# Kernel tuning notes

Measured on AMD Instinct MI355X. Metric: run time of the kernel, lower is better.

## Reference

```python
import jax, jax.numpy as jnp
import numpy as np

N_NODES = 100000
N_EDGES = 1600000
IN_FEATS = 128
H_FEATS = 64
NUM_CLASSES = 40
NEG_SLOPE = 0.2  # DGL GATConv default


def gat_layer(x, src, dst, W, attn_l, attn_r, bias, n_nodes):
    # x: [N, din]; W: [din, dout]; attn_l/r, bias: [dout]
    feat = x @ W                                   # [N, dout]
    el = feat @ attn_l                             # [N]
    er = feat @ attn_r                             # [N]
    e = jax.nn.leaky_relu(el[src] + er[dst], NEG_SLOPE)  # [E]
    # segment softmax over destination nodes (numerically stable)
    m = jax.ops.segment_max(e, dst, num_segments=n_nodes)   # [N]
    ee = jnp.exp(e - m[dst])                                 # [E]
    s = jax.ops.segment_sum(ee, dst, num_segments=n_nodes)  # [N]
    alpha = ee / s[dst]                                      # [E]
    out = jax.ops.segment_sum(alpha[:, None] * feat[src], dst,
                              num_segments=n_nodes)          # [N, dout]
    return out + bias


def setup_inputs() -> dict:
    key = jax.random.key(0)
    ks = jax.random.split(key, 12)
    in_feat = jax.random.normal(ks[0], (N_NODES, IN_FEATS), dtype=jnp.float32)
    src = jax.random.randint(ks[1], (N_EDGES,), 0, N_NODES, dtype=jnp.int32)
    dst = jax.random.randint(ks[2], (N_EDGES,), 0, N_NODES, dtype=jnp.int32)
    def glorot(k, shape):
        fan = sum(shape)
        return jax.random.normal(k, shape, dtype=jnp.float32) * jnp.sqrt(2.0 / fan)
    W1 = glorot(ks[3], (IN_FEATS, H_FEATS))
    al1 = glorot(ks[4], (H_FEATS,)) 
    ar1 = glorot(ks[5], (H_FEATS,))
    b1 = jnp.zeros((H_FEATS,), jnp.float32)
    W2 = glorot(ks[6], (H_FEATS, NUM_CLASSES))
    al2 = glorot(ks[7], (NUM_CLASSES,))
    ar2 = glorot(ks[8], (NUM_CLASSES,))
    b2 = jnp.zeros((NUM_CLASSES,), jnp.float32)
    return {"in_feat": in_feat, "src": src, "dst": dst,
            "W1": W1, "al1": al1, "ar1": ar1, "b1": b1,
            "W2": W2, "al2": al2, "ar2": ar2, "b2": b2}


def reference(in_feat, src, dst, W1, al1, ar1, b1, W2, al2, ar2, b2):
    h = gat_layer(in_feat, src, dst, W1, al1, ar1, b1, N_NODES)  # gat1
    h = jax.nn.elu(h)                                            # F.elu
    h = gat_layer(h, src, dst, W2, al2, ar2, b2, N_NODES)        # gat2
    return h  # [N, num_classes]
```

## Files before the change

### kernel.cpp

```cpp
#include <hip/hip_runtime.h>

#define N_NODES 100000
#define N_EDGES 1600000
#define DB_SHIFT 9
#define DB_SIZE 512
#define NDB 196
#define DB_CAP 10240

constexpr float NEG_SLOPE = 0.2f;

__device__ __forceinline__ float leaky(float x) { return x > 0.f ? x : NEG_SLOPE * x; }

__device__ __forceinline__ float bflo(unsigned u) { return __uint_as_float(u << 16); }
__device__ __forceinline__ float bfhi(unsigned u) { return __uint_as_float(u & 0xffff0000u); }

__device__ __forceinline__ void bfsplit(float x, short& h, short& l) {
    unsigned u = __float_as_uint(x);
    h = (short)(u >> 16);
    float res = x - __uint_as_float(u & 0xffff0000u);
    unsigned r = __float_as_uint(res);
    r = (r + 0x7fffu + ((r >> 16) & 1u)) >> 16;
    l = (short)r;
}

__global__ __launch_bounds__(256) void partition_dst_kernel(
        const int* __restrict__ src, const int* __restrict__ dst,
        int* __restrict__ db_cursor, unsigned* __restrict__ staged, int E) {
    __shared__ unsigned pay_s[4096];
    __shared__ unsigned stage[4096];
    __shared__ unsigned char bktA[4096];
    __shared__ unsigned char bkt_s[4096];
    __shared__ unsigned hist[256];
    __shared__ unsigned scanb[256];
    __shared__ unsigned baseg[256];
    __shared__ unsigned cnt[256];
    int tid = threadIdx.x;
    int e0 = blockIdx.x * 4096;
    hist[tid] = 0;
    cnt[tid] = 0;
    __syncthreads();
#pragma unroll
    for (int k = 0; k < 16; ++k) {
        int idx = k * 256 + tid;
        int i = e0 + idx;
        if (i < E) {
            int d = dst[i];
            unsigned b = (unsigned)d >> DB_SHIFT;
            pay_s[idx] = (((unsigned)d & (DB_SIZE - 1)) << 17) | (unsigned)src[i];
            bktA[idx] = (unsigned char)b;
            atomicAdd(&hist[b], 1u);
        }
    }
    __syncthreads();
    unsigned v = hist[tid];
    scanb[tid] = v;
    __syncthreads();
    for (int off = 1; off < 256; off <<= 1) {
        unsigned t = (tid >= off) ? scanb[tid - off] : 0;
        __syncthreads();
        scanb[tid] += t;
        __syncthreads();
    }
    unsigned excl = scanb[tid] - v;
    __syncthreads();
    scanb[tid] = excl;
    if (tid < NDB)
        baseg[tid] = (unsigned)(tid * DB_CAP) + (unsigned)atomicAdd(&db_cursor[tid], (int)v);
    __syncthreads();
#pragma unroll
    for (int k = 0; k < 16; ++k) {
        int idx = k * 256 + tid;
        int i = e0 + idx;
        if (i < E) {
            unsigned b = bktA[idx];
            unsigned slot = scanb[b] + atomicAdd(&cnt[b], 1u);
            stage[slot] = pay_s[idx];
            bkt_s[slot] = (unsigned char)b;
        }
    }
    __syncthreads();
    int total = min(4096, E - e0);
    for (int j = tid; j < total; j += 256) {
        unsigned b = bkt_s[j];
        unsigned addr = baseg[b] + ((unsigned)j - scanb[b]);
        staged[addr] = stage[j];
    }
}

__global__ __launch_bounds__(256) void bucket_scan_kernel(const int* __restrict__ db_cursor,
                                                          int* __restrict__ db_base,
                                                          int* __restrict__ row_ptr, int N, int E) {
    __shared__ int sh[256];
    int tid = threadIdx.x;
    int c = (tid < NDB) ? db_cursor[tid] : 0;
    sh[tid] = c;
    __syncthreads();
    for (int off = 1; off < 256; off <<= 1) {
        int t = (tid >= off) ? sh[tid - off] : 0;
        __syncthreads();
        sh[tid] += t;
        __syncthreads();
    }
    if (tid < NDB) db_base[tid] = sh[tid] - c;
    if (tid == 0) row_ptr[N] = E;
}

__global__ __launch_bounds__(256) void bucket_sort_kernel(
        const unsigned* __restrict__ staged, const int* __restrict__ db_cnt,
        const int* __restrict__ db_base, int* __restrict__ csr_src,
        int* __restrict__ row_ptr, int N) {
    __shared__ unsigned pay[DB_CAP];
    __shared__ int sorted[DB_CAP];
    __shared__ int hist[DB_SIZE];
    __shared__ int excl[DB_SIZE];
    __shared__ int psum[256];
    int tid = threadIdx.x;
    int k = blockIdx.x;
    int cnt = db_cnt[k];
    int base = db_base[k];
    for (int i = tid; i < DB_SIZE; i += 256) hist[i] = 0;
    __syncthreads();
    for (int j = tid; j < cnt; j += 256) {
        unsigned p = staged[(size_t)k * DB_CAP + j];
        pay[j] = p;
        atomicAdd(&hist[p >> 17], 1);
    }
    __syncthreads();
    int s = hist[2 * tid] + hist[2 * tid + 1];
    psum[tid] = s;
    __syncthreads();
    for (int off = 1; off < 256; off <<= 1) {
        int t = (tid >= off) ? psum[tid - off] : 0;
        __syncthreads();
        psum[tid] += t;
        __syncthreads();
    }
    int e0 = psum[tid] - s;
    excl[2 * tid] = e0;
    excl[2 * tid + 1] = e0 + hist[2 * tid];
    __syncthreads();
    for (int i = tid; i < DB_SIZE; i += 256) {
        int d = k * DB_SIZE + i;
        if (d < N) row_ptr[d] = base + excl[i];
    }
    for (int i = tid; i < DB_SIZE; i += 256) hist[i] = 0;
    __syncthreads();
    for (int j = tid; j < cnt; j += 256) {
        unsigned p = pay[j];
        int dl = (int)(p >> 17);
        int pos = excl[dl] + atomicAdd(&hist[dl], 1);
        sorted[pos] = (int)(p & 0x1FFFFu);
    }
    __syncthreads();
    for (int j = tid; j < cnt; j += 256) csr_src[base + j] = sorted[j];
}

__global__ void wconv_kernel(const float* __restrict__ W, int K, int Nw, int Npad,
                             unsigned short* __restrict__ WTh, unsigned short* __restrict__ WTl) {
    int idx = blockIdx.x * 256 + threadIdx.x;
    if (idx >= Npad * K) return;
    int n = idx / K, k = idx % K;
    float x = (n < Nw) ? W[(size_t)k * Nw + n] : 0.f;
    short h, l;
    bfsplit(x, h, l);
    WTh[idx] = (unsigned short)h;
    WTl[idx] = (unsigned short)l;
}

template <int DIN, int NOUT, int NTILES, int OSTR>
__global__ __launch_bounds__(256) void gemm_mfma_kernel(
        const float* __restrict__ X,
        const unsigned short* __restrict__ WTh, const unsigned short* __restrict__ WTl,
        const float* __restrict__ al, const float* __restrict__ ar,
        unsigned short* __restrict__ featb, float* __restrict__ el,
        float* __restrict__ er, int N) {
    constexpr int KT = DIN / 32;
    using frag = __attribute__((ext_vector_type(8))) short;
    using accv = __attribute__((ext_vector_type(4))) float;

    int lane = threadIdx.x & 63;
    int wid = threadIdx.x >> 6;
    int r0 = (blockIdx.x * 4 + wid) * 16;
    if (r0 >= N) return;
    int m = lane & 15;
    int quad = lane >> 4;
    int row = r0 + m;
    bool rok = row < N;
    const float* xrow = X + (size_t)(rok ? row : 0) * DIN;

    frag ah[KT], alo[KT];
#pragma unroll
    for (int kt = 0; kt < KT; ++kt) {
        float xv[8];
        if (rok) {
            float4 a0 = *reinterpret_cast<const float4*>(xrow + kt * 32 + quad * 8);
            float4 a1 = *reinterpret_cast<const float4*>(xrow + kt * 32 + quad * 8 + 4);
            xv[0] = a0.x; xv[1] = a0.y; xv[2] = a0.z; xv[3] = a0.w;
            xv[4] = a1.x; xv[5] = a1.y; xv[6] = a1.z; xv[7] = a1.w;
        } else {
#pragma unroll
            for (int j = 0; j < 8; ++j) xv[j] = 0.f;
        }
#pragma unroll
        for (int j = 0; j < 8; ++j) {
            short h, l;
            bfsplit(xv[j], h, l);
            ah[kt][j] = h;
            alo[kt][j] = l;
        }
    }

    accv acc[NTILES];
#pragma unroll
    for (int nt = 0; nt < NTILES; ++nt) acc[nt] = (accv){0.f, 0.f, 0.f, 0.f};

#pragma unroll
    for (int nt = 0; nt < NTILES; ++nt) {
        const unsigned short* bh_base = WTh + (size_t)(nt * 16 + m) * DIN;
        const unsigned short* bl_base = WTl + (size_t)(nt * 16 + m) * DIN;
#pragma unroll
        for (int kt = 0; kt < KT; ++kt) {
            frag bh = *reinterpret_cast<const frag*>(bh_base + kt * 32 + quad * 8);
            frag bl = *reinterpret_cast<const frag*>(bl_base + kt * 32 + quad * 8);
            acc[nt] = __builtin_amdgcn_mfma_f32_16x16x32_bf16(ah[kt], bh, acc[nt], 0, 0, 0);
            acc[nt] = __builtin_amdgcn_mfma_f32_16x16x32_bf16(ah[kt], bl, acc[nt], 0, 0, 0);
            acc[nt] = __builtin_amdgcn_mfma_f32_16x16x32_bf16(alo[kt], bh, acc[nt], 0, 0, 0);
        }
    }

    float pel[4] = {0.f, 0.f, 0.f, 0.f};
    float per[4] = {0.f, 0.f, 0.f, 0.f};
#pragma unroll
    for (int nt = 0; nt < NTILES; ++nt) {
        int n = nt * 16 + m;
        float av = (n < NOUT) ? al[n] : 0.f;
        float rv = (n < NOUT) ? ar[n] : 0.f;
#pragma unroll
        for (int reg = 0; reg < 4; ++reg) {
            float v = acc[nt][reg];
            pel[reg] += v * av;
            per[reg] += v * rv;
            int grow = r0 + quad * 4 + reg;
            if (grow < N && n < NOUT) {
                unsigned u = __float_as_uint(v);
                u = (u + 0x7fffu + ((u >> 16) & 1u)) >> 16;
                featb[(size_t)grow * OSTR + n] = (unsigned short)u;
            }
        }
    }
#pragma unroll
    for (int o = 1; o < 16; o <<= 1) {
#pragma unroll
        for (int reg = 0; reg < 4; ++reg) {
            pel[reg] += __shfl_xor(pel[reg], o, 64);
            per[reg] += __shfl_xor(per[reg], o, 64);
        }
    }
    if (m == 0) {
#pragma unroll
        for (int reg = 0; reg < 4; ++reg) {
            int grow = r0 + quad * 4 + reg;
            if (grow < N) { el[grow] = pel[reg]; er[grow] = per[reg]; }
        }
    }
}

template <int DOUT, int FSTR, int OSTR, bool ELU>
__global__ void agg_kernel(const int* __restrict__ row_ptr, const int* __restrict__ csr_src,
                           const float* __restrict__ el, const float* __restrict__ er,
                           const unsigned short* __restrict__ featb,
                           const float* __restrict__ bias, float* __restrict__ outp, int N) {
    int lane = threadIdx.x & 63;
    int n = blockIdx.x * (blockDim.x >> 6) + (threadIdx.x >> 6);
    if (n >= N) return;
    int beg = row_ptr[n];
    int end = row_ptr[n + 1];
    int deg = end - beg;
    float ern = er[n];

    constexpr int G2 = DOUT / 4;

    if (deg <= 64) {
        int s = 0;
        float e = -1e30f;
        bool act = lane < deg;
        if (act) {
            s = csr_src[beg + lane];
            e = leaky(el[s] + ern);
        }
        float m = e;
#pragma unroll
        for (int o = 32; o > 0; o >>= 1) m = fmaxf(m, __shfl_xor(m, o, 64));
        float ee = act ? __expf(e - m) : 0.f;
        float ssum = ee;
#pragma unroll
        for (int o = 32; o > 0; o >>= 1) ssum += __shfl_xor(ssum, o, 64);

        int g = lane >> 4;
        int cl = lane & 15;
        float4 acc = make_float4(0.f, 0.f, 0.f, 0.f);
        int niter = (deg + 3) >> 2;
        for (int i = 0; i < niter; i += 2) {
            int e0 = 4 * i + g;
            int e1 = e0 + 4;
            float w0 = __shfl(ee, e0 & 63, 64);
            int s0 = __shfl(s, e0 & 63, 64);
            float w1 = __shfl(ee, e1 & 63, 64);
            int s1 = __shfl(s, e1 & 63, 64);
            if (e0 >= deg) w0 = 0.f;
            if (e1 >= deg) w1 = 0.f;
            if (cl < G2) {
                uint2 q0 = *(reinterpret_cast<const uint2*>(featb + (size_t)s0 * FSTR) + cl);
                uint2 q1 = *(reinterpret_cast<const uint2*>(featb + (size_t)s1 * FSTR) + cl);
                acc.x += w0 * bflo(q0.x) + w1 * bflo(q1.x);
                acc.y += w0 * bfhi(q0.x) + w1 * bfhi(q1.x);
                acc.z += w0 * bflo(q0.y) + w1 * bflo(q1.y);
                acc.w += w0 * bfhi(q0.y) + w1 * bfhi(q1.y);
            }
        }
#pragma unroll
        for (int o = 16; o <= 32; o <<= 1) {
            acc.x += __shfl_xor(acc.x, o, 64);
            acc.y += __shfl_xor(acc.y, o, 64);
            acc.z += __shfl_xor(acc.z, o, 64);
            acc.w += __shfl_xor(acc.w, o, 64);
        }
        if (g == 0 && cl < G2) {
            float inv = (deg > 0) ? 1.f / ssum : 0.f;
            const float4 b4 = reinterpret_cast<const float4*>(bias)[cl];
            float4 o4;
            o4.x = acc.x * inv + b4.x;
            o4.y = acc.y * inv + b4.y;
            o4.z = acc.z * inv + b4.z;
            o4.w = acc.w * inv + b4.w;
            if (ELU) {
                o4.x = o4.x > 0.f ? o4.x : (__expf(o4.x) - 1.f);
                o4.y = o4.y > 0.f ? o4.y : (__expf(o4.y) - 1.f);
                o4.z = o4.z > 0.f ? o4.z : (__expf(o4.z) - 1.f);
                o4.w = o4.w > 0.f ? o4.w : (__expf(o4.w) - 1.f);
            }
            *reinterpret_cast<float4*>(outp + (size_t)n * OSTR + 4 * cl) = o4;
        }
        return;
    }

    float m = -1e30f;
    for (int j = beg + lane; j < end; j += 64) {
        float e = leaky(el[csr_src[j]] + ern);
        m = fmaxf(m, e);
    }
#pragma unroll
    for (int o = 32; o > 0; o >>= 1) m = fmaxf(m, __shfl_xor(m, o, 64));

    float ssum = 0.f;
    float acc = 0.f;
    for (int base = beg; base < end; base += 64) {
        int j = base + lane;
        int cnt = min(64, end - base);
        int s = (lane < cnt) ? csr_src[j] : 0;
        float ee = 0.f;
        if (lane < cnt) {
            float e = leaky(el[s] + ern);
            ee = __expf(e - m);
        }
        ssum += ee;
        for (int t = 0; t < cnt; ++t) {
            float w = __shfl(ee, t, 64);
            int sj = __shfl(s, t, 64);
            if (lane < DOUT)
                acc += w * __uint_as_float(((unsigned)featb[(size_t)sj * FSTR + lane]) << 16);
        }
    }
#pragma unroll
    for (int o = 32; o > 0; o >>= 1) ssum += __shfl_xor(ssum, o, 64);

    if (lane < DOUT) {
        float o = acc / ssum + bias[lane];
        if (ELU) o = (o > 0.f) ? o : (__expf(o) - 1.f);
        outp[(size_t)n * OSTR + lane] = o;
    }
}

extern "C" void kernel_launch(void* const* d_in, const int* in_sizes, int n_in,
                              void* d_out, int out_size, void* d_ws, size_t ws_size,
                              hipStream_t stream) {
    const float* in_feat = (const float*)d_in[0];
    const int* src = (const int*)d_in[1];
    const int* dst = (const int*)d_in[2];
    const float* W1 = (const float*)d_in[3];
    const float* al1 = (const float*)d_in[4];
    const float* ar1 = (const float*)d_in[5];
    const float* b1 = (const float*)d_in[6];
    const float* W2 = (const float*)d_in[7];
    const float* al2 = (const float*)d_in[8];
    const float* ar2 = (const float*)d_in[9];
    const float* b2 = (const float*)d_in[10];
    float* out = (float*)d_out;

    const int N = N_NODES, E = N_EDGES;

    size_t off = 0;
    auto carve = [&](size_t bytes) {
        void* p = (char*)d_ws + off;
        off += (bytes + 255) & ~(size_t)255;
        return p;
    };
    unsigned short* featb = (unsigned short*)carve((size_t)N * 64 * 2);
    float* el    = (float*)carve((size_t)N * 4);
    float* er    = (float*)carve((size_t)N * 4);
    int* row_ptr = (int*)carve((size_t)(N + 1) * 4);
    int* csr_src = (int*)carve((size_t)E * 4);
    int* db_cursor = (int*)carve((size_t)NDB * 4);
    int* db_base   = (int*)carve((size_t)NDB * 4);
    unsigned short* W1Th = (unsigned short*)carve((size_t)64 * 128 * 2);
    unsigned short* W1Tl = (unsigned short*)carve((size_t)64 * 128 * 2);
    unsigned short* W2Th = (unsigned short*)carve((size_t)48 * 64 * 2);
    unsigned short* W2Tl = (unsigned short*)carve((size_t)48 * 64 * 2);
    size_t offH = off;
    float* h = (float*)carve((size_t)N * 64 * 4);
    size_t off_end = off;
    off = offH;
    unsigned* staged = (unsigned*)carve((size_t)NDB * DB_CAP * 4);
    off = off_end;

    hipMemsetAsync(db_cursor, 0, (size_t)NDB * 4, stream);

    partition_dst_kernel<<<(E + 4095) / 4096, 256, 0, stream>>>(src, dst, db_cursor, staged, E);
    bucket_scan_kernel<<<1, 256, 0, stream>>>(db_cursor, db_base, row_ptr, N, E);
    bucket_sort_kernel<<<NDB, 256, 0, stream>>>(staged, db_cursor, db_base, csr_src, row_ptr, N);

    wconv_kernel<<<(64 * 128 + 255) / 256, 256, 0, stream>>>(W1, 128, 64, 64, W1Th, W1Tl);
    wconv_kernel<<<(48 * 64 + 255) / 256, 256, 0, stream>>>(W2, 64, 40, 48, W2Th, W2Tl);

    int agrid = (N + 3) / 4;
    int ggrid = (N + 63) / 64;

    gemm_mfma_kernel<128, 64, 4, 64>
        <<<ggrid, 256, 0, stream>>>(in_feat, W1Th, W1Tl, al1, ar1, featb, el, er, N);
    agg_kernel<64, 64, 64, true><<<agrid, 256, 0, stream>>>(row_ptr, csr_src, el, er, featb, b1, h, N);

    gemm_mfma_kernel<64, 40, 3, 48>
        <<<ggrid, 256, 0, stream>>>(h, W2Th, W2Tl, al2, ar2, featb, el, er, N);
    agg_kernel<40, 48, 40, false><<<agrid, 256, 0, stream>>>(row_ptr, csr_src, el, er, featb, b2, out, N);
}
```

Measured before the change: 295.9 us.

## Fuse edge partition with layer-1 GEMM and fold scans into fewer launches

Merges the dst-bucket partition kernel and the first-layer MFMA GEMM into one launch whose blocks branch by index, so the two independent stages run concurrently. The bucket prefix scan moves into every bucket_sort block, and the memset plus both weight conversions are folded into a single kernel. Partition chunk size is halved to 2048 edges, giving more blocks. This removes several small launches and serialization gaps, at the cost of redundant scans per block and a higher shared-memory and register footprint for the fused kernel, which may lower occupancy of the GEMM half.

Result: faster. 288.6 us (-2.5%).

```diff
diff --git a/kernel.cpp b/kernel.cpp
--- a/kernel.cpp
+++ b/kernel.cpp
@@ -6,6 +6,9 @@
 #define DB_SIZE 512
 #define NDB 196
 #define DB_CAP 10240
+#define PART_EDGES 2048
+#define NPART ((N_EDGES + PART_EDGES - 1) / PART_EDGES)
+#define NGEMM1 ((N_NODES + 63) / 64)
 
 constexpr float NEG_SLOPE = 0.2f;
 
@@ -23,153 +26,32 @@
     l = (short)r;
 }
 
-__global__ __launch_bounds__(256) void partition_dst_kernel(
-        const int* __restrict__ src, const int* __restrict__ dst,
-        int* __restrict__ db_cursor, unsigned* __restrict__ staged, int E) {
-    __shared__ unsigned pay_s[4096];
-    __shared__ unsigned stage[4096];
-    __shared__ unsigned char bktA[4096];
-    __shared__ unsigned char bkt_s[4096];
-    __shared__ unsigned hist[256];
-    __shared__ unsigned scanb[256];
-    __shared__ unsigned baseg[256];
-    __shared__ unsigned cnt[256];
-    int tid = threadIdx.x;
-    int e0 = blockIdx.x * 4096;
-    hist[tid] = 0;
-    cnt[tid] = 0;
-    __syncthreads();
-#pragma unroll
-    for (int k = 0; k < 16; ++k) {
-        int idx = k * 256 + tid;
-        int i = e0 + idx;
-        if (i < E) {
-            int d = dst[i];
-            unsigned b = (unsigned)d >> DB_SHIFT;
-            pay_s[idx] = (((unsigned)d & (DB_SIZE - 1)) << 17) | (unsigned)src[i];
-            bktA[idx] = (unsigned char)b;
-            atomicAdd(&hist[b], 1u);
-        }
-    }
-    __syncthreads();
-    unsigned v = hist[tid];
-    scanb[tid] = v;
-    __syncthreads();
-    for (int off = 1; off < 256; off <<= 1) {
-        unsigned t = (tid >= off) ? scanb[tid - off] : 0;
-        __syncthreads();
-        scanb[tid] += t;
-        __syncthreads();
-    }
-    unsigned excl = scanb[tid] - v;
-    __syncthreads();
-    scanb[tid] = excl;
-    if (tid < NDB)
-        baseg[tid] = (unsigned)(tid * DB_CAP) + (unsigned)atomicAdd(&db_cursor[tid], (int)v);
-    __syncthreads();
-#pragma unroll
-    for (int k = 0; k < 16; ++k) {
-        int idx = k * 256 + tid;
-        int i = e0 + idx;
-        if (i < E) {
-            unsigned b = bktA[idx];
-            unsigned slot = scanb[b] + atomicAdd(&cnt[b], 1u);
-            stage[slot] = pay_s[idx];
-            bkt_s[slot] = (unsigned char)b;
-        }
-    }
-    __syncthreads();
-    int total = min(4096, E - e0);
-    for (int j = tid; j < total; j += 256) {
-        unsigned b = bkt_s[j];
-        unsigned addr = baseg[b] + ((unsigned)j - scanb[b]);
-        staged[addr] = stage[j];
-    }
-}
-
-__global__ __launch_bounds__(256) void bucket_scan_kernel(const int* __restrict__ db_cursor,
-                                                          int* __restrict__ db_base,
-                                                          int* __restrict__ row_ptr, int N, int E) {
-    __shared__ int sh[256];
-    int tid = threadIdx.x;
-    int c = (tid < NDB) ? db_cursor[tid] : 0;
-    sh[tid] = c;
-    __syncthreads();
-    for (int off = 1; off < 256; off <<= 1) {
-        int t = (tid >= off) ? sh[tid - off] : 0;
-        __syncthreads();
-        sh[tid] += t;
-        __syncthreads();
-    }
-    if (tid < NDB) db_base[tid] = sh[tid] - c;
-    if (tid == 0) row_ptr[N] = E;
-}
-
-__global__ __launch_bounds__(256) void bucket_sort_kernel(
-        const unsigned* __restrict__ staged, const int* __restrict__ db_cnt,
-        const int* __restrict__ db_base, int* __restrict__ csr_src,
-        int* __restrict__ row_ptr, int N) {
-    __shared__ unsigned pay[DB_CAP];
-    __shared__ int sorted[DB_CAP];
-    __shared__ int hist[DB_SIZE];
-    __shared__ int excl[DB_SIZE];
-    __shared__ int psum[256];
-    int tid = threadIdx.x;
-    int k = blockIdx.x;
-    int cnt = db_cnt[k];
-    int base = db_base[k];
-    for (int i = tid; i < DB_SIZE; i += 256) hist[i] = 0;
-    __syncthreads();
-    for (int j = tid; j < cnt; j += 256) {
-        unsigned p = staged[(size_t)k * DB_CAP + j];
-        pay[j] = p;
-        atomicAdd(&hist[p >> 17], 1);
-    }
-    __syncthreads();
-    int s = hist[2 * tid] + hist[2 * tid + 1];
-    psum[tid] = s;
-    __syncthreads();
-    for (int off = 1; off < 256; off <<= 1) {
-        int t = (tid >= off) ? psum[tid - off] : 0;
-        __syncthreads();
-        psum[tid] += t;
-        __syncthreads();
-    }
-    int e0 = psum[tid] - s;
-    excl[2 * tid] = e0;
-    excl[2 * tid + 1] = e0 + hist[2 * tid];
-    __syncthreads();
-    for (int i = tid; i < DB_SIZE; i += 256) {
-        int d = k * DB_SIZE + i;
-        if (d < N) row_ptr[d] = base + excl[i];
-    }
-    for (int i = tid; i < DB_SIZE; i += 256) hist[i] = 0;
-    __syncthreads();
-    for (int j = tid; j < cnt; j += 256) {
-        unsigned p = pay[j];
-        int dl = (int)(p >> 17);
-        int pos = excl[dl] + atomicAdd(&hist[dl], 1);
-        sorted[pos] = (int)(p & 0x1FFFFu);
-    }
-    __syncthreads();
-    for (int j = tid; j < cnt; j += 256) csr_src[base + j] = sorted[j];
-}
-
-__global__ void wconv_kernel(const float* __restrict__ W, int K, int Nw, int Npad,
-                             unsigned short* __restrict__ WTh, unsigned short* __restrict__ WTl) {
+__global__ void wconv2_kernel(const float* __restrict__ W1, const float* __restrict__ W2,
+                              unsigned short* __restrict__ W1Th, unsigned short* __restrict__ W1Tl,
+                              unsigned short* __restrict__ W2Th, unsigned short* __restrict__ W2Tl,
+                              int* __restrict__ db_cursor) {
     int idx = blockIdx.x * 256 + threadIdx.x;
-    if (idx >= Npad * K) return;
-    int n = idx / K, k = idx % K;
-    float x = (n < Nw) ? W[(size_t)k * Nw + n] : 0.f;
-    short h, l;
-    bfsplit(x, h, l);
-    WTh[idx] = (unsigned short)h;
-    WTl[idx] = (unsigned short)l;
+    if (blockIdx.x == 0 && threadIdx.x < NDB) db_cursor[threadIdx.x] = 0;
+    if (idx < 64 * 128) {
+        int n = idx / 128, k = idx % 128;
+        short h, l;
+        bfsplit(W1[(size_t)k * 64 + n], h, l);
+        W1Th[idx] = (unsigned short)h;
+        W1Tl[idx] = (unsigned short)l;
+    } else if (idx < 64 * 128 + 48 * 64) {
+        int j = idx - 64 * 128;
+        int n = j / 64, k = j % 64;
+        float x = (n < 40) ? W2[(size_t)k * 40 + n] : 0.f;
+        short h, l;
+        bfsplit(x, h, l);
+        W2Th[j] = (unsigned short)h;
+        W2Tl[j] = (unsigned short)l;
+    }
 }
 
 template <int DIN, int NOUT, int NTILES, int OSTR>
-__global__ __launch_bounds__(256) void gemm_mfma_kernel(
-        const float* __restrict__ X,
+__device__ __forceinline__ void gemm_mfma_body(
+        int bid, const float* __restrict__ X,
         const unsigned short* __restrict__ WTh, const unsigned short* __restrict__ WTl,
         const float* __restrict__ al, const float* __restrict__ ar,
         unsigned short* __restrict__ featb, float* __restrict__ el,
@@ -180,7 +62,7 @@
 
     int lane = threadIdx.x & 63;
     int wid = threadIdx.x >> 6;
-    int r0 = (blockIdx.x * 4 + wid) * 16;
+    int r0 = (bid * 4 + wid) * 16;
     if (r0 >= N) return;
     int m = lane & 15;
     int quad = lane >> 4;
@@ -263,6 +145,149 @@
             if (grow < N) { el[grow] = pel[reg]; er[grow] = per[reg]; }
         }
     }
+}
+
+__global__ __launch_bounds__(256) void fusedA_kernel(
+        const int* __restrict__ src, const int* __restrict__ dst,
+        int* __restrict__ db_cursor, unsigned* __restrict__ staged, int E,
+        const float* __restrict__ X,
+        const unsigned short* __restrict__ W1Th, const unsigned short* __restrict__ W1Tl,
+        const float* __restrict__ al, const float* __restrict__ ar,
+        unsigned short* __restrict__ featb, float* __restrict__ el,
+        float* __restrict__ er, int N) {
+    if (blockIdx.x < NPART) {
+        __shared__ unsigned pay_s[PART_EDGES];
+        __shared__ unsigned stage[PART_EDGES];
+        __shared__ unsigned char bktA[PART_EDGES];
+        __shared__ unsigned char bkt_s[PART_EDGES];
+        __shared__ unsigned hist[256];
+        __shared__ unsigned scanb[256];
+        __shared__ unsigned baseg[256];
+        __shared__ unsigned cnt[256];
+        int tid = threadIdx.x;
+        int e0 = blockIdx.x * PART_EDGES;
+        hist[tid] = 0;
+        cnt[tid] = 0;
+        __syncthreads();
+#pragma unroll
+        for (int k = 0; k < PART_EDGES / 256; ++k) {
+            int idx = k * 256 + tid;
+            int i = e0 + idx;
+            if (i < E) {
+                int d = dst[i];
+                unsigned b = (unsigned)d >> DB_SHIFT;
+                pay_s[idx] = (((unsigned)d & (DB_SIZE - 1)) << 17) | (unsigned)src[i];
+                bktA[idx] = (unsigned char)b;
+                atomicAdd(&hist[b], 1u);
+            }
+        }
+        __syncthreads();
+        unsigned v = hist[tid];
+        scanb[tid] = v;
+        __syncthreads();
+        for (int off = 1; off < 256; off <<= 1) {
+            unsigned t = (tid >= off) ? scanb[tid - off] : 0;
+            __syncthreads();
+            scanb[tid] += t;
+            __syncthreads();
+        }
+        unsigned excl = scanb[tid] - v;
+        __syncthreads();
+        scanb[tid] = excl;
+        if (tid < NDB)
+            baseg[tid] = (unsigned)(tid * DB_CAP) + (unsigned)atomicAdd(&db_cursor[tid], (int)v);
+        __syncthreads();
+#pragma unroll
+        for (int k = 0; k < PART_EDGES / 256; ++k) {
+            int idx = k * 256 + tid;
+            int i = e0 + idx;
+            if (i < E) {
+                unsigned b = bktA[idx];
+                unsigned slot = scanb[b] + atomicAdd(&cnt[b], 1u);
+                stage[slot] = pay_s[idx];
+                bkt_s[slot] = (unsigned char)b;
+            }
+        }
+        __syncthreads();
+        int total = min(PART_EDGES, E - e0);
+        for (int j = tid; j < total; j += 256) {
+            unsigned b = bkt_s[j];
+            unsigned addr = baseg[b] + ((unsigned)j - scanb[b]);
+            staged[addr] = stage[j];
+        }
+    } else {
+        gemm_mfma_body<128, 64, 4, 64>(blockIdx.x - NPART, X, W1Th, W1Tl, al, ar, featb, el, er, N);
+    }
+}
+
+__global__ __launch_bounds__(256) void bucket_sort_kernel(
+        const unsigned* __restrict__ staged, const int* __restrict__ db_cursor,
+        int* __restrict__ csr_src, int* __restrict__ row_ptr, int N, int E) {
+    __shared__ unsigned pay[DB_CAP];
+    __shared__ int sorted[DB_CAP];
+    __shared__ int hist[DB_SIZE];
+    __shared__ int excl[DB_SIZE];
+    __shared__ int psum[256];
+    __shared__ int scn[256];
+    int tid = threadIdx.x;
+    int k = blockIdx.x;
+    int c = (tid < NDB) ? db_cursor[tid] : 0;
+    scn[tid] = c;
+    __syncthreads();
+    for (int off = 1; off < 256; off <<= 1) {
+        int t = (tid >= off) ? scn[tid - off] : 0;
+        __syncthreads();
+        scn[tid] += t;
+        __syncthreads();
+    }
+    int cnt = db_cursor[k];
+    int base = scn[k] - cnt;
+    if (k == 0 && tid == 0) row_ptr[N] = E;
+
+    for (int i = tid; i < DB_SIZE; i += 256) hist[i] = 0;
+    __syncthreads();
+    for (int j = tid; j < cnt; j += 256) {
+        unsigned p = staged[(size_t)k * DB_CAP + j];
+        pay[j] = p;
+        atomicAdd(&hist[p >> 17], 1);
+    }
+    __syncthreads();
+    int s = hist[2 * tid] + hist[2 * tid + 1];
+    psum[tid] = s;
+    __syncthreads();
+    for (int off = 1; off < 256; off <<= 1) {
+        int t = (tid >= off) ? psum[tid - off] : 0;
+        __syncthreads();
+        psum[tid] += t;
+        __syncthreads();
+    }
+    int e0 = psum[tid] - s;
+    excl[2 * tid] = e0;
+    excl[2 * tid + 1] = e0 + hist[2 * tid];
+    __syncthreads();
+    for (int i = tid; i < DB_SIZE; i += 256) {
+        int d = k * DB_SIZE + i;
+        if (d < N) row_ptr[d] = base + excl[i];
+    }
+    for (int i = tid; i < DB_SIZE; i += 256) hist[i] = 0;
+    __syncthreads();
+    for (int j = tid; j < cnt; j += 256) {
+        unsigned p = pay[j];
+        int dl = (int)(p >> 17);
+        int pos = excl[dl] + atomicAdd(&hist[dl], 1);
+        sorted[pos] = (int)(p & 0x1FFFFu);
+    }
+    __syncthreads();
+    for (int j = tid; j < cnt; j += 256) csr_src[base + j] = sorted[j];
+}
+
+__global__ __launch_bounds__(256) void gemm2_kernel(
+        const float* __restrict__ X,
+        const unsigned short* __restrict__ WTh, const unsigned short* __restrict__ WTl,
+        const float* __restrict__ al, const float* __restrict__ ar,
+        unsigned short* __restrict__ featb, float* __restrict__ el,
+        float* __restrict__ er, int N) {
+    gemm_mfma_body<64, 40, 3, 48>(blockIdx.x, X, WTh, WTl, al, ar, featb, el, er, N);
 }
 
 template <int DOUT, int FSTR, int OSTR, bool ELU>
@@ -411,7 +436,6 @@
     int* row_ptr = (int*)carve((size_t)(N + 1) * 4);
     int* csr_src = (int*)carve((size_t)E * 4);
     int* db_cursor = (int*)carve((size_t)NDB * 4);
-    int* db_base   = (int*)carve((size_t)NDB * 4);
     unsigned short* W1Th = (unsigned short*)carve((size_t)64 * 128 * 2);
     unsigned short* W1Tl = (unsigned short*)carve((size_t)64 * 128 * 2);
     unsigned short* W2Th = (unsigned short*)carve((size_t)48 * 64 * 2);
@@ -423,23 +447,20 @@
     unsigned* staged = (unsigned*)carve((size_t)NDB * DB_CAP * 4);
     off = off_end;
 
-    hipMemsetAsync(db_cursor, 0, (size_t)NDB * 4, stream);
-
-    partition_dst_kernel<<<(E + 4095) / 4096, 256, 0, stream>>>(src, dst, db_cursor, staged, E);
-    bucket_scan_kernel<<<1, 256, 0, stream>>>(db_cursor, db_base, row_ptr, N, E);
-    bucket_sort_kernel<<<NDB, 256, 0, stream>>>(staged, db_cursor, db_base, csr_src, row_ptr, N);
-
-    wconv_kernel<<<(64 * 128 + 255) / 256, 256, 0, stream>>>(W1, 128, 64, 64, W1Th, W1Tl);
-    wconv_kernel<<<(48 * 64 + 255) / 256, 256, 0, stream>>>(W2, 64, 40, 48, W2Th, W2Tl);
+    wconv2_kernel<<<(64 * 128 + 48 * 64 + 255) / 256, 256, 0, stream>>>(
+        W1, W2, W1Th, W1Tl, W2Th, W2Tl, db_cursor);
+
+    fusedA_kernel<<<NPART + NGEMM1, 256, 0, stream>>>(
+        src, dst, db_cursor, staged, E,
+        in_feat, W1Th, W1Tl, al1, ar1, featb, el, er, N);
+
+    bucket_sort_kernel<<<NDB, 256, 0, stream>>>(staged, db_cursor, csr_src, row_ptr, N, E);
 
     int agrid = (N + 3) / 4;
-    int ggrid = (N + 63) / 64;
-
-    gemm_mfma_kernel<128, 64, 4, 64>
-        <<<ggrid, 256, 0, stream>>>(in_feat, W1Th, W1Tl, al1, ar1, featb, el, er, N);
+
     agg_kernel<64, 64, 64, true><<<agrid, 256, 0, stream>>>(row_ptr, csr_src, el, er, featb, b1, h, N);
 
-    gemm_mfma_kernel<64, 40, 3, 48>
-        <<<ggrid, 256, 0, stream>>>(h, W2Th, W2Tl, al2, ar2, featb, el, er, N);
+    gemm2_kernel<<<(N + 63) / 64, 256, 0, stream>>>(h, W2Th, W2Tl, al2, ar2, featb, el, er, N);
+
     agg_kernel<40, 48, 40, false><<<agrid, 256, 0, stream>>>(row_ptr, csr_src, el, er, featb, b2, out, N);
 }
```
